# Optimization experiments

Hardware: AMD Instinct MI355X
Metric: run time of the kernel (lower is better)

Reference implementation:

```python
import jax, jax.numpy as jnp
import numpy as np

V, B, C, D, H, W = 5, 2, 32, 48, 128, 160


def setup_inputs() -> dict:
    key = jax.random.key(0)
    k1, k2, k3, k4 = jax.random.split(key, 4)
    features = jax.random.normal(k1, (V, B, C, H, W), jnp.float32)
    # Intrinsics (shared) and per-view extrinsics (identity rotation + small translation)
    K = np.eye(4, dtype=np.float32)
    K[0, 0] = 200.0; K[1, 1] = 200.0; K[0, 2] = W / 2.0; K[1, 2] = H / 2.0
    projs = np.zeros((B, V, 2, 4, 4), np.float32)
    for v in range(V):
        E = np.eye(4, dtype=np.float32)
        E[0, 3] = 0.1 * v
        E[1, 3] = 0.05 * v
        projs[:, v, 0] = E
        projs[:, v, 1] = K
    proj_matrices = jnp.asarray(projs)
    # Per-pixel depth sweep in [2, 10] with slight pixelwise perturbation
    d = jnp.linspace(2.0, 10.0, D, dtype=jnp.float32)
    depth_samples = jnp.broadcast_to(d[None, :, None, None], (B, D, H, W)) * (
        1.0 + 0.01 * jax.random.uniform(k2, (B, 1, H, W), jnp.float32))
    view_weights = jax.random.uniform(k3, (B, V - 1, H, W), jnp.float32, 0.1, 1.0)
    w_reg = 0.1 * jax.random.normal(k4, (C,), jnp.float32)
    b_reg = jnp.zeros((1,), jnp.float32)
    return {"features": features, "proj_matrices": proj_matrices,
            "depth_samples": depth_samples, "view_weights": view_weights,
            "w_reg": w_reg, "b_reg": b_reg}


def _bilinear_sample(img, px, py):
    # img: (C, H, W); px, py: (D, H, W) pixel coords. Zeros padding, align_corners=True.
    Cc, Hh, Ww = img.shape
    x0 = jnp.floor(px); y0 = jnp.floor(py)
    wx1 = px - x0; wx0 = 1.0 - wx1
    wy1 = py - y0; wy0 = 1.0 - wy1

    def gather(ix, iy, wgt):
        valid = (ix >= 0) & (ix <= Ww - 1) & (iy >= 0) & (iy <= Hh - 1)
        ixc = jnp.clip(ix, 0, Ww - 1).astype(jnp.int32)
        iyc = jnp.clip(iy, 0, Hh - 1).astype(jnp.int32)
        v = img[:, iyc, ixc]  # (C, D, H, W)
        return v * (wgt * valid)[None]

    return (gather(x0, y0, wx0 * wy0) + gather(x0 + 1, y0, wx1 * wy0)
            + gather(x0, y0 + 1, wx0 * wy1) + gather(x0 + 1, y0 + 1, wx1 * wy1))


def homo_warping(src_fea, src_proj, ref_proj, depth):
    # src_fea: (B,C,H,W); projs: (B,4,4); depth: (B,D,H,W) -> warped (B,C,D,H,W)
    Bn, Cc, Hh, Ww = src_fea.shape
    Dn = depth.shape[1]
    proj = src_proj @ jnp.linalg.inv(ref_proj)
    rot = proj[:, :3, :3]
    tr = proj[:, :3, 3]
    yy, xx = jnp.meshgrid(jnp.arange(Hh, dtype=src_fea.dtype),
                          jnp.arange(Ww, dtype=src_fea.dtype), indexing='ij')
    xyz = jnp.stack([xx.ravel(), yy.ravel(), jnp.ones(Hh * Ww, src_fea.dtype)])  # (3, HW)
    rot_xyz = jnp.einsum('bij,jn->bin', rot, xyz)  # (B, 3, HW)
    pxyz = rot_xyz[:, :, None, :] * depth.reshape(Bn, 1, Dn, Hh * Ww) + tr[:, :, None, None]
    z = pxyz[:, 2]
    valid = z > 1e-3
    zs = jnp.where(valid, z, 1.0)
    px = jnp.where(valid, pxyz[:, 0] / zs, -1e4).reshape(Bn, Dn, Hh, Ww)
    py = jnp.where(valid, pxyz[:, 1] / zs, -1e4).reshape(Bn, Dn, Hh, Ww)
    return jax.vmap(_bilinear_sample)(src_fea, px, py)


def _combined_proj(p):
    # p: (B, 2, 4, 4); new[:, :3, :4] = K[:3,:3] @ E[:3,:4]
    new = p[:, 0]
    return new.at[:, :3, :4].set(jnp.einsum('bij,bjk->bik', p[:, 1, :3, :3], p[:, 0, :3, :4]))


def reference(features, proj_matrices, depth_samples, view_weights, w_reg, b_reg):
    ref_fea = features[0]  # (B, C, H, W)
    Bn, Cc, Hh, Ww = ref_fea.shape
    Dn = depth_samples.shape[1]
    ref_proj_new = _combined_proj(proj_matrices[:, 0])
    vol_sum = jnp.zeros((Bn, Cc, Dn, Hh, Ww), ref_fea.dtype)
    wsum = jnp.full((Bn, 1, 1, Hh, Ww), 1e-5, ref_fea.dtype)
    nsrc = features.shape[0] - 1
    for i in range(nsrc):  # small fixed view loop
        src_proj_new = _combined_proj(proj_matrices[:, i + 1])
        warped = homo_warping(features[i + 1], src_proj_new, ref_proj_new, depth_samples)
        warped = warped * ref_fea[:, :, None]  # similarity volume
        w = view_weights[:, i][:, None, None]  # (B, 1, 1, H, W)
        vol_sum = vol_sum + warped * w
        wsum = wsum + w
    volume_aggregated = vol_sum / wsum
    # cost_reg_net stand-in: 1x1x1 conv over channels -> (B, D, H, W)
    prob_volume_pre = jnp.einsum('bcdhw,c->bdhw', volume_aggregated, w_reg) + b_reg
    prob_volume = jax.nn.softmax(prob_volume_pre, axis=1)
    depth = jnp.sum(prob_volume * depth_samples, axis=1)
    return (depth, jax.lax.stop_gradient(view_weights), prob_volume, volume_aggregated)
```

## Files before the change

### kernel.cpp

```cpp
#include <hip/hip_runtime.h>
#include <hip/hip_bf16.h>
#include <math.h>

#define V_ 5
#define B_ 2
#define C_ 32
#define D_ 48
#define H_ 128
#define W_ 160
#define NSRC 4
#define HW_ (H_ * W_)
#define DHW_ ((size_t)D_ * H_ * W_)
#define BHW_ (B_ * H_ * W_)
#define TOTAL_BDHW (B_ * D_ * H_ * W_)

#define NB_VOL (B_ * (H_ / 4) * (W_ / 16) * D_)
#define NB_VOL8 (NB_VOL / 8)

typedef __attribute__((ext_vector_type(2))) float f32x2;

__device__ __forceinline__ void combined_proj(const float* p, double* P) {
    double E[16], K[16];
    for (int i = 0; i < 16; ++i) { E[i] = (double)p[i]; K[i] = (double)p[16 + i]; }
    for (int i = 0; i < 16; ++i) P[i] = E[i];
    for (int r = 0; r < 3; ++r)
        for (int c = 0; c < 4; ++c) {
            double s = 0.0;
            for (int j = 0; j < 3; ++j) s += K[r * 4 + j] * E[j * 4 + c];
            P[r * 4 + c] = s;
        }
}

__device__ void invert4(const double* A, double* out) {
    double M[4][8];
    for (int r = 0; r < 4; ++r)
        for (int c = 0; c < 4; ++c) {
            M[r][c] = A[r * 4 + c];
            M[r][c + 4] = (r == c) ? 1.0 : 0.0;
        }
    for (int col = 0; col < 4; ++col) {
        int piv = col;
        double best = fabs(M[col][col]);
        for (int r = col + 1; r < 4; ++r) {
            double v = fabs(M[r][col]);
            if (v > best) { best = v; piv = r; }
        }
        if (piv != col)
            for (int c = 0; c < 8; ++c) {
                double t = M[col][c]; M[col][c] = M[piv][c]; M[piv][c] = t;
            }
        double s = 1.0 / M[col][col];
        for (int c = 0; c < 8; ++c) M[col][c] *= s;
        for (int r = 0; r < 4; ++r)
            if (r != col) {
                double f = M[r][col];
                if (f != 0.0)
                    for (int c = 0; c < 8; ++c) M[r][c] -= f * M[col][c];
            }
    }
    for (int r = 0; r < 4; ++r)
        for (int c = 0; c < 4; ++c) out[r * 4 + c] = M[r][c + 4];
}

__global__ void proj_kernel(const float* __restrict__ pm, float* __restrict__ out) {
    int t = threadIdx.x;
    if (t >= B_ * NSRC) return;
    int b = t / NSRC, i = t % NSRC;
    double Pref[16], Psrc[16];
    combined_proj(pm + (size_t)((b * V_ + 0) * 2) * 16, Pref);
    combined_proj(pm + (size_t)((b * V_ + (i + 1)) * 2) * 16, Psrc);
    double inv[16];
    invert4(Pref, inv);
    double M[16];
    for (int r = 0; r < 4; ++r)
        for (int c = 0; c < 4; ++c) {
            double s = 0.0;
            for (int j = 0; j < 4; ++j) s += Psrc[r * 4 + j] * inv[j * 4 + c];
            M[r * 4 + c] = s;
        }
    float* o = out + t * 12;
    o[0] = (float)M[0];  o[1] = (float)M[1];  o[2] = (float)M[2];
    o[3] = (float)M[4];  o[4] = (float)M[5];  o[5] = (float)M[6];
    o[6] = (float)M[8];  o[7] = (float)M[9];  o[8] = (float)M[10];
    o[9] = (float)M[3];  o[10] = (float)M[7]; o[11] = (float)M[11];
}

__global__ __launch_bounds__(256) void transpose_bf16_kernel(
    const float* __restrict__ in, __hip_bfloat16* __restrict__ outT) {
    __shared__ float tile[32][33];
    int ibh = blockIdx.x;
    int w0 = blockIdx.y * 32;
    int h = ibh % H_;
    int ib = ibh / H_;
    int i = ib / B_, b = ib % B_;
    int tx = threadIdx.x, ty = threadIdx.y;
    const float* src = in + ((size_t)((i + 1) * B_ + b) * C_) * HW_ + (size_t)h * W_ + w0;
#pragma unroll
    for (int cs = 0; cs < 32; cs += 8)
        tile[cs + ty][tx] = src[(size_t)(cs + ty) * HW_ + tx];
    __syncthreads();
    __hip_bfloat16* dst = outT + ((size_t)ib * HW_ + (size_t)h * W_ + w0) * C_;
#pragma unroll
    for (int wv = 0; wv < 32; wv += 8)
        dst[(size_t)(wv + ty) * C_ + tx] = __float2bfloat16(tile[tx][wv + ty]);
}

__global__ __launch_bounds__(256, 4) void vol_split_kernel(
    const __hip_bfloat16* __restrict__ featT, const float* __restrict__ features,
    const float* __restrict__ depth_samples, const float* __restrict__ view_weights,
    const float* __restrict__ w_reg, const float* __restrict__ b_reg,
    const float* __restrict__ projs, float* __restrict__ out_vol,
    float* __restrict__ out_pv) {
    __shared__ float lds[NSRC * 64 * 12];

    int bid = blockIdx.x;
    int lid = (bid & 7) * NB_VOL8 + (bid >> 3);
    int d = lid % D_;
    int r = lid / D_;
    int wg = r % (W_ / 16);
    r /= (W_ / 16);
    int h4 = r % (H_ / 4);
    int b = r / (H_ / 4);

    int tix = threadIdx.x;

    {
        int p = tix & 63;
        int v = tix >> 6;
        int w = wg * 16 + (p & 15);
        int h = h4 * 4 + (p >> 4);
        int pix = ((b * D_ + d) * H_ + h) * W_ + w;
        float dep = depth_samples[pix];
        float vw = view_weights[((size_t)(b * NSRC + v) * H_ + h) * W_ + w];
        const float* pr = projs + (b * NSRC + v) * 12;
        float xf = (float)w, yf = (float)h;
        float rx = pr[0] * xf + pr[1] * yf + pr[2];
        float ry = pr[3] * xf + pr[4] * yf + pr[5];
        float rz = pr[6] * xf + pr[7] * yf + pr[8];
        float pxn = rx * dep + pr[9];
        float pyn = ry * dep + pr[10];
        float z = rz * dep + pr[11];
        bool valid = z > 0.001f;
        float zr = __builtin_amdgcn_rcpf(valid ? z : 1.f);
        float px = valid ? pxn * zr : -10000.f;
        float py = valid ? pyn * zr : -10000.f;

        float x0f = floorf(px), y0f = floorf(py);
        float wx1 = px - x0f, wx0 = 1.f - wx1;
        float wy1 = py - y0f, wy0 = 1.f - wy1;
        bool vx0 = (x0f >= 0.f) && (x0f <= (float)(W_ - 1));
        bool vx1 = (x0f >= -1.f) && (x0f <= (float)(W_ - 2));
        bool vy0 = (y0f >= 0.f) && (y0f <= (float)(H_ - 1));
        bool vy1 = (y0f >= -1.f) && (y0f <= (float)(H_ - 2));
        int ix0 = (int)fminf(fmaxf(x0f, 0.f), (float)(W_ - 1));
        int ix1 = (int)fminf(fmaxf(x0f + 1.f, 0.f), (float)(W_ - 1));
        int iy0 = (int)fminf(fmaxf(y0f, 0.f), (float)(H_ - 1));
        int iy1 = (int)fminf(fmaxf(y0f + 1.f, 0.f), (float)(H_ - 1));
        float w00 = wx0 * wy0 * ((vx0 && vy0) ? vw : 0.f);
        float w10 = wx1 * wy0 * ((vx1 && vy0) ? vw : 0.f);
        float w01 = wx0 * wy1 * ((vx0 && vy1) ? vw : 0.f);
        float w11 = wx1 * wy1 * ((vx1 && vy1) ? vw : 0.f);

        int o00 = (iy0 * W_ + ix0) << 6;
        int o10 = (iy0 * W_ + ix1) << 6;
        int o01 = (iy1 * W_ + ix0) << 6;
        int o11 = (iy1 * W_ + ix1) << 6;

        float* row = lds + (size_t)((v << 6) + p) * 12;
        *(float4*)row = make_float4(w00, w10, w01, w11);
        *(int4*)(row + 4) = make_int4(o00, o10, o01, o11);
        row[8] = vw;
    }
    __syncthreads();

    int w16 = tix & 15;
    int c4 = (tix >> 4) & 3;
    int hg = tix >> 6;
    int p = w16 + 16 * hg;
    int h = h4 * 4 + hg;
    int w = wg * 16 + w16;
    int c0 = c4 * 8;
    int c16 = c4 * 16;

    float4 wv4[NSRC];
    int4 ov[NSRC];
    float vws[NSRC];
#pragma unroll
    for (int v = 0; v < NSRC; ++v) {
        const float* row = lds + (size_t)((v << 6) + p) * 12;
        wv4[v] = *(const float4*)row;
        ov[v] = *(const int4*)(row + 4);
        vws[v] = row[8];
    }
    float wsum = 1e-5f + vws[0] + vws[1] + vws[2] + vws[3];

    uint4 u[NSRC][4];
#pragma unroll
    for (int v = 0; v < NSRC; ++v) {
        const char* fv = (const char*)(featT + (size_t)(v * B_ + b) * HW_ * C_) + c16;
        u[v][0] = *(const uint4*)(fv + ov[v].x);
        u[v][1] = *(const uint4*)(fv + ov[v].y);
        u[v][2] = *(const uint4*)(fv + ov[v].z);
        u[v][3] = *(const uint4*)(fv + ov[v].w);
    }

    const float* refp = features + ((size_t)b * C_ + c0) * HW_ + (size_t)h * W_ + w;
    float refv[8];
#pragma unroll
    for (int k = 0; k < 8; ++k) refv[k] = refp[(size_t)k * HW_];

    __builtin_amdgcn_sched_barrier(0);

    f32x2 acc[4];
#pragma unroll
    for (int j = 0; j < 4; ++j) acc[j] = (f32x2){0.f, 0.f};

#define ACCPK(word, j, wgt)                                              \
    {                                                                    \
        f32x2 t;                                                         \
        t.x = __uint_as_float((word) << 16);                             \
        t.y = __uint_as_float((word) & 0xffff0000u);                     \
        acc[j] += t * (wgt);                                             \
    }
#pragma unroll
    for (int v = 0; v < NSRC; ++v) {
        f32x2 wv;
#define ACCTAP(uu, wcomp)                                                \
        wv = (f32x2){wcomp, wcomp};                                      \
        ACCPK((uu).x, 0, wv)                                             \
        ACCPK((uu).y, 1, wv)                                             \
        ACCPK((uu).z, 2, wv)                                             \
        ACCPK((uu).w, 3, wv)
        ACCTAP(u[v][0], wv4[v].x)
        ACCTAP(u[v][1], wv4[v].y)
        ACCTAP(u[v][2], wv4[v].z)
        ACCTAP(u[v][3], wv4[v].w)
#undef ACCTAP
    }
#undef ACCPK

    float inv_wsum = __builtin_amdgcn_rcpf(wsum);
    int pix_idx = ((b * D_ + d) * H_ + h) * W_ + w;
    size_t obase = (size_t)b * C_ * DHW_ + (size_t)d * HW_ + (size_t)h * W_ + w;
    float4 wr0 = *(const float4*)(w_reg + c0);
    float4 wr1 = *(const float4*)(w_reg + c0 + 4);
    float wrr[8] = {wr0.x, wr0.y, wr0.z, wr0.w, wr1.x, wr1.y, wr1.z, wr1.w};
    float pv = 0.f;
#pragma unroll
    for (int k = 0; k < 8; ++k) {
        float vc = refv[k] * acc[k >> 1][k & 1] * inv_wsum;
        __builtin_nontemporal_store(vc, &out_vol[obase + (size_t)(c0 + k) * DHW_]);
        pv += vc * wrr[k];
    }
    pv += __shfl_xor(pv, 16, 64);
    pv += __shfl_xor(pv, 32, 64);
    if (c4 == 0) out_pv[pix_idx] = pv + b_reg[0];
}

__global__ __launch_bounds__(256) void vol_fallback_kernel(
    const float* __restrict__ feat, const float* __restrict__ depth_samples,
    const float* __restrict__ view_weights, const float* __restrict__ w_reg,
    const float* __restrict__ b_reg, const float* __restrict__ projs,
    float* __restrict__ out_vol, float* __restrict__ out_pv) {
    int tid = blockIdx.x * 256 + threadIdx.x;
    if (tid >= TOTAL_BDHW) return;
    int w = tid % W_;
    int t2 = tid / W_;
    int h = t2 % H_;
    t2 /= H_;
    int d = t2 % D_;
    int b = t2 / D_;

    float xf = (float)w, yf = (float)h;
    float dep = depth_samples[tid];
    float s[C_];
#pragma unroll
    for (int c = 0; c < C_; ++c) s[c] = 0.f;
    float wsum = 1e-5f;

    for (int i = 0; i < NSRC; ++i) {
        float vw = view_weights[((size_t)(b * NSRC + i) * H_ + h) * W_ + w];
        wsum += vw;
        const float* pr = projs + (b * NSRC + i) * 12;
        float rx = pr[0] * xf + pr[1] * yf + pr[2];
        float ry = pr[3] * xf + pr[4] * yf + pr[5];
        float rz = pr[6] * xf + pr[7] * yf + pr[8];
        float pxn = rx * dep + pr[9];
        float pyn = ry * dep + pr[10];
        float z = rz * dep + pr[11];
        bool valid = z > 0.001f;
        float zs = valid ? z : 1.f;
        float px = valid ? pxn / zs : -10000.f;
        float py = valid ? pyn / zs : -10000.f;
        float x0f = floorf(px), y0f = floorf(py);
        float x1f = x0f + 1.f, y1f = y0f + 1.f;
        float wx1 = px - x0f, wx0 = 1.f - wx1;
        float wy1 = py - y0f, wy0 = 1.f - wy1;
        bool vx0 = (x0f >= 0.f) && (x0f <= (float)(W_ - 1));
        bool vx1 = (x1f >= 0.f) && (x1f <= (float)(W_ - 1));
        bool vy0 = (y0f >= 0.f) && (y0f <= (float)(H_ - 1));
        bool vy1 = (y1f >= 0.f) && (y1f <= (float)(H_ - 1));
        int ix0 = (int)fminf(fmaxf(x0f, 0.f), (float)(W_ - 1));
        int ix1 = (int)fminf(fmaxf(x1f, 0.f), (float)(W_ - 1));
        int iy0 = (int)fminf(fmaxf(y0f, 0.f), (float)(H_ - 1));
        int iy1 = (int)fminf(fmaxf(y1f, 0.f), (float)(H_ - 1));
        float w00 = wx0 * wy0 * ((vx0 && vy0) ? vw : 0.f);
        float w10 = wx1 * wy0 * ((vx1 && vy0) ? vw : 0.f);
        float w01 = wx0 * wy1 * ((vx0 && vy1) ? vw : 0.f);
        float w11 = wx1 * wy1 * ((vx1 && vy1) ? vw : 0.f);
// ... 37 lines not shown
#pragma unroll
    for (int d = 0; d < D_; ++d) {
        p[d] = pv[base + (size_t)d * HW_];
        m = fmaxf(m, p[d]);
    }
    float ssum = 0.f;
#pragma unroll
    for (int d = 0; d < D_; ++d) {
        p[d] = expf(p[d] - m);
        ssum += p[d];
    }
    float inv = 1.f / ssum;
    float dep = 0.f;
#pragma unroll
    for (int d = 0; d < D_; ++d) {
        float pr = p[d] * inv;
        pv[base + (size_t)d * HW_] = pr;
        dep += pr * ds[base + (size_t)d * HW_];
    }
    out_depth[tid] = dep;
#pragma unroll
    for (int k = 0; k < NSRC; ++k)
        out_vw[tid + k * BHW_] = vw[tid + k * BHW_];
}

extern "C" void kernel_launch(void* const* d_in, const int* in_sizes, int n_in,
                              void* d_out, int out_size, void* d_ws, size_t ws_size,
                              hipStream_t stream) {
    const float* features = (const float*)d_in[0];
    const float* pm       = (const float*)d_in[1];
    const float* dsamp    = (const float*)d_in[2];
    const float* vweights = (const float*)d_in[3];
    const float* w_reg    = (const float*)d_in[4];
    const float* b_reg    = (const float*)d_in[5];

    float* out = (float*)d_out;
    float* out_depth = out;
    float* out_vw    = out + 40960;
    float* out_prob  = out + 204800;
    float* out_vol   = out + 2170880;

    float* wsf   = (float*)d_ws;
    float* projb = wsf;
    __hip_bfloat16* featT = (__hip_bfloat16*)(wsf + 128);

    size_t need = 512 + (size_t)NSRC * B_ * HW_ * C_ * sizeof(__hip_bfloat16);
    bool chlast = (ws_size >= need);

    hipLaunchKernelGGL(proj_kernel, dim3(1), dim3(64), 0, stream, pm, projb);

    if (chlast) {
        hipLaunchKernelGGL(transpose_bf16_kernel, dim3(NSRC * B_ * H_, W_ / 32),
                           dim3(32, 8), 0, stream, features, featT);
        hipLaunchKernelGGL(vol_split_kernel, dim3(NB_VOL), dim3(256), 0, stream,
                           featT, features, dsamp, vweights, w_reg, b_reg, projb,
                           out_vol, out_prob);
    } else {
        hipLaunchKernelGGL(vol_fallback_kernel, dim3((TOTAL_BDHW + 255) / 256),
                           dim3(256), 0, stream, features, dsamp, vweights, w_reg,
                           b_reg, projb, out_vol, out_prob);
    }

    hipLaunchKernelGGL(finalize_kernel, dim3(BHW_ / 256), dim3(256), 0, stream,
                       dsamp, vweights, out_depth, out_vw, out_prob);
}
```

Before: 169.7 us.

## Loop over depth inside each block with double-buffered LDS sampling rows

Replaces the one-block-per-depth-slice volume kernel with a kernel where each block handles half the depth range for a 4x16 pixel tile. Per-pixel setup (projection ray, view weight, reference features, w_reg, weight-sum reciprocal) is hoisted out of the depth loop and reused. Sampling rows for the next depth are computed into a second LDS buffer while the current depth is gathered. The grid shrinks from roughly 30k blocks to 1280, which cuts redundant loads and block launch overhead but lowers parallelism and adds a barrier per depth step.

```diff
diff --git a/kernel.cpp b/kernel.cpp
--- a/kernel.cpp
+++ b/kernel.cpp
@@ -14,8 +14,9 @@
 #define BHW_ (B_ * H_ * W_)
 #define TOTAL_BDHW (B_ * D_ * H_ * W_)
 
-#define NB_VOL (B_ * (H_ / 4) * (W_ / 16) * D_)
-#define NB_VOL8 (NB_VOL / 8)
+#define DHALF (D_ / 2)
+#define NB_DLOOP (B_ * (H_ / 4) * (W_ / 16) * 2)
+#define NB_DLOOP8 (NB_DLOOP / 8)
 
 typedef __attribute__((ext_vector_type(2))) float f32x2;
 
@@ -105,156 +106,195 @@
         dst[(size_t)(wv + ty) * C_ + tx] = __float2bfloat16(tile[tx][wv + ty]);
 }
 
-__global__ __launch_bounds__(256, 4) void vol_split_kernel(
+__device__ __forceinline__ void make_row(float dep, float rx, float ry, float rz,
+                                         float t9, float t10, float t11, float vw,
+                                         float* __restrict__ row) {
+    float pxn = rx * dep + t9;
+    float pyn = ry * dep + t10;
+    float z = rz * dep + t11;
+    bool valid = z > 0.001f;
+    float zr = __builtin_amdgcn_rcpf(valid ? z : 1.f);
+    float px = valid ? pxn * zr : -10000.f;
+    float py = valid ? pyn * zr : -10000.f;
+
+    float x0f = floorf(px), y0f = floorf(py);
+    float wx1 = px - x0f, wx0 = 1.f - wx1;
+    float wy1 = py - y0f, wy0 = 1.f - wy1;
+    bool vx0 = (x0f >= 0.f) && (x0f <= (float)(W_ - 1));
+    bool vx1 = (x0f >= -1.f) && (x0f <= (float)(W_ - 2));
+    bool vy0 = (y0f >= 0.f) && (y0f <= (float)(H_ - 1));
+    bool vy1 = (y0f >= -1.f) && (y0f <= (float)(H_ - 2));
+    int ix0 = (int)fminf(fmaxf(x0f, 0.f), (float)(W_ - 1));
+    int ix1 = (int)fminf(fmaxf(x0f + 1.f, 0.f), (float)(W_ - 1));
+    int iy0 = (int)fminf(fmaxf(y0f, 0.f), (float)(H_ - 1));
+    int iy1 = (int)fminf(fmaxf(y0f + 1.f, 0.f), (float)(H_ - 1));
+    float w00 = wx0 * wy0 * ((vx0 && vy0) ? vw : 0.f);
+    float w10 = wx1 * wy0 * ((vx1 && vy0) ? vw : 0.f);
+    float w01 = wx0 * wy1 * ((vx0 && vy1) ? vw : 0.f);
+    float w11 = wx1 * wy1 * ((vx1 && vy1) ? vw : 0.f);
+
+    int o00 = (iy0 * W_ + ix0) << 6;
+    int o10 = (iy0 * W_ + ix1) << 6;
+    int o01 = (iy1 * W_ + ix0) << 6;
+    int o11 = (iy1 * W_ + ix1) << 6;
+
+    *(float4*)row = make_float4(w00, w10, w01, w11);
+    *(int4*)(row + 4) = make_int4(o00, o10, o01, o11);
+    row[8] = vw;
+}
+
+__global__ __launch_bounds__(256, 4) void vol_dloop_kernel(
     const __hip_bfloat16* __restrict__ featT, const float* __restrict__ features,
     const float* __restrict__ depth_samples, const float* __restrict__ view_weights,
     const float* __restrict__ w_reg, const float* __restrict__ b_reg,
     const float* __restrict__ projs, float* __restrict__ out_vol,
     float* __restrict__ out_pv) {
-    __shared__ float lds[NSRC * 64 * 12];
+    __shared__ float lds[2][NSRC * 64 * 12];
 
     int bid = blockIdx.x;
-    int lid = (bid & 7) * NB_VOL8 + (bid >> 3);
-    int d = lid % D_;
-    int r = lid / D_;
-    int wg = r % (W_ / 16);
-    r /= (W_ / 16);
-    int h4 = r % (H_ / 4);
-    int b = r / (H_ / 4);
+    int lid = (bid & 7) * NB_DLOOP8 + (bid >> 3);
+    int dhalf = lid & 1;
+    int t = lid >> 1;
+    int wg = t % (W_ / 16);
+    t /= (W_ / 16);
+    int h4 = t % (H_ / 4);
+    int b = t / (H_ / 4);
+    int d0 = dhalf * DHALF;
 
     int tix = threadIdx.x;
 
-    {
-        int p = tix & 63;
-        int v = tix >> 6;
-        int w = wg * 16 + (p & 15);
-        int h = h4 * 4 + (p >> 4);
-        int pix = ((b * D_ + d) * H_ + h) * W_ + w;
-        float dep = depth_samples[pix];
-        float vw = view_weights[((size_t)(b * NSRC + v) * H_ + h) * W_ + w];
-        const float* pr = projs + (b * NSRC + v) * 12;
-        float xf = (float)w, yf = (float)h;
-        float rx = pr[0] * xf + pr[1] * yf + pr[2];
-        float ry = pr[3] * xf + pr[4] * yf + pr[5];
-        float rz = pr[6] * xf + pr[7] * yf + pr[8];
-        float pxn = rx * dep + pr[9];
-        float pyn = ry * dep + pr[10];
-        float z = rz * dep + pr[11];
-        bool valid = z > 0.001f;
-        float zr = __builtin_amdgcn_rcpf(valid ? z : 1.f);
-        float px = valid ? pxn * zr : -10000.f;
-        float py = valid ? pyn * zr : -10000.f;
-
-        float x0f = floorf(px), y0f = floorf(py);
-        float wx1 = px - x0f, wx0 = 1.f - wx1;
-        float wy1 = py - y0f, wy0 = 1.f - wy1;
-        bool vx0 = (x0f >= 0.f) && (x0f <= (float)(W_ - 1));
-        bool vx1 = (x0f >= -1.f) && (x0f <= (float)(W_ - 2));
-        bool vy0 = (y0f >= 0.f) && (y0f <= (float)(H_ - 1));
-        bool vy1 = (y0f >= -1.f) && (y0f <= (float)(H_ - 2));
-        int ix0 = (int)fminf(fmaxf(x0f, 0.f), (float)(W_ - 1));
-        int ix1 = (int)fminf(fmaxf(x0f + 1.f, 0.f), (float)(W_ - 1));
-        int iy0 = (int)fminf(fmaxf(y0f, 0.f), (float)(H_ - 1));
-        int iy1 = (int)fminf(fmaxf(y0f + 1.f, 0.f), (float)(H_ - 1));
-        float w00 = wx0 * wy0 * ((vx0 && vy0) ? vw : 0.f);
-        float w10 = wx1 * wy0 * ((vx1 && vy0) ? vw : 0.f);
-        float w01 = wx0 * wy1 * ((vx0 && vy1) ? vw : 0.f);
-        float w11 = wx1 * wy1 * ((vx1 && vy1) ? vw : 0.f);
-
-        int o00 = (iy0 * W_ + ix0) << 6;
-        int o10 = (iy0 * W_ + ix1) << 6;
-        int o01 = (iy1 * W_ + ix0) << 6;
-        int o11 = (iy1 * W_ + ix1) << 6;
-
-        float* row = lds + (size_t)((v << 6) + p) * 12;
-        *(float4*)row = make_float4(w00, w10, w01, w11);
-        *(int4*)(row + 4) = make_int4(o00, o10, o01, o11);
-        row[8] = vw;
-    }
-    __syncthreads();
+    int p1 = tix & 63;
+    int v1 = tix >> 6;
+    int w1 = wg * 16 + (p1 & 15);
+    int h1 = h4 * 4 + (p1 >> 4);
+    const float* pr = projs + (b * NSRC + v1) * 12;
+    float xf = (float)w1, yf = (float)h1;
+    float rx = pr[0] * xf + pr[1] * yf + pr[2];
+    float ry = pr[3] * xf + pr[4] * yf + pr[5];
+    float rz = pr[6] * xf + pr[7] * yf + pr[8];
+    float t9 = pr[9], t10 = pr[10], t11 = pr[11];
+    float vw1 = view_weights[((size_t)(b * NSRC + v1) * H_ + h1) * W_ + w1];
+    int dspix1 = (b * D_) * HW_ + h1 * W_ + w1;
+    float* row0 = &lds[0][(size_t)((v1 << 6) + p1) * 12];
+    float* row1 = &lds[1][(size_t)((v1 << 6) + p1) * 12];
 
     int w16 = tix & 15;
     int c4 = (tix >> 4) & 3;
     int hg = tix >> 6;
-    int p = w16 + 16 * hg;
-    int h = h4 * 4 + hg;
-    int w = wg * 16 + w16;
+    int p2 = w16 + 16 * hg;
+    int h2 = h4 * 4 + hg;
+    int w2 = wg * 16 + w16;
     int c0 = c4 * 8;
-    int c16 = c4 * 16;
-
-    float4 wv4[NSRC];
-    int4 ov[NSRC];
-    float vws[NSRC];
-#pragma unroll
-    for (int v = 0; v < NSRC; ++v) {
-        const float* row = lds + (size_t)((v << 6) + p) * 12;
-        wv4[v] = *(const float4*)row;
-        ov[v] = *(const int4*)(row + 4);
-        vws[v] = row[8];
-    }
-    float wsum = 1e-5f + vws[0] + vws[1] + vws[2] + vws[3];
-
-    uint4 u[NSRC][4];
-#pragma unroll
-    for (int v = 0; v < NSRC; ++v) {
-        const char* fv = (const char*)(featT + (size_t)(v * B_ + b) * HW_ * C_) + c16;
-        u[v][0] = *(const uint4*)(fv + ov[v].x);
-        u[v][1] = *(const uint4*)(fv + ov[v].y);
-        u[v][2] = *(const uint4*)(fv + ov[v].z);
-        u[v][3] = *(const uint4*)(fv + ov[v].w);
-    }
-
-    const float* refp = features + ((size_t)b * C_ + c0) * HW_ + (size_t)h * W_ + w;
+    int c16b = c4 * 16;
+    const char* fv0 = (const char*)(featT + (size_t)(0 * B_ + b) * HW_ * C_) + c16b;
+    const char* fv1 = (const char*)(featT + (size_t)(1 * B_ + b) * HW_ * C_) + c16b;
+    const char* fv2 = (const char*)(featT + (size_t)(2 * B_ + b) * HW_ * C_) + c16b;
+    const char* fv3 = (const char*)(featT + (size_t)(3 * B_ + b) * HW_ * C_) + c16b;
+    const float* rbase0 = &lds[0][(size_t)p2 * 12];
+    const float* rbase1 = &lds[1][(size_t)p2 * 12];
+
+    const float* refp = features + ((size_t)b * C_ + c0) * HW_ + (size_t)h2 * W_ + w2;
     float refv[8];
 #pragma unroll
     for (int k = 0; k < 8; ++k) refv[k] = refp[(size_t)k * HW_];
-
-    __builtin_amdgcn_sched_barrier(0);
-
-    f32x2 acc[4];
-#pragma unroll
-    for (int j = 0; j < 4; ++j) acc[j] = (f32x2){0.f, 0.f};
-
-#define ACCPK(word, j, wgt)                                              \
-    {                                                                    \
-        f32x2 t;                                                         \
-        t.x = __uint_as_float((word) << 16);                             \
-        t.y = __uint_as_float((word) & 0xffff0000u);                     \
-        acc[j] += t * (wgt);                                             \
-    }
-#pragma unroll
-    for (int v = 0; v < NSRC; ++v) {
-        f32x2 wv;
-#define ACCTAP(uu, wcomp)                                                \
-        wv = (f32x2){wcomp, wcomp};                                      \
-        ACCPK((uu).x, 0, wv)                                             \
-        ACCPK((uu).y, 1, wv)                                             \
-        ACCPK((uu).z, 2, wv)                                             \
-        ACCPK((uu).w, 3, wv)
-        ACCTAP(u[v][0], wv4[v].x)
-        ACCTAP(u[v][1], wv4[v].y)
-        ACCTAP(u[v][2], wv4[v].z)
-        ACCTAP(u[v][3], wv4[v].w)
-#undef ACCTAP
-    }
-#undef ACCPK
-
-    float inv_wsum = __builtin_amdgcn_rcpf(wsum);
-    int pix_idx = ((b * D_ + d) * H_ + h) * W_ + w;
-    size_t obase = (size_t)b * C_ * DHW_ + (size_t)d * HW_ + (size_t)h * W_ + w;
     float4 wr0 = *(const float4*)(w_reg + c0);
     float4 wr1 = *(const float4*)(w_reg + c0 + 4);
     float wrr[8] = {wr0.x, wr0.y, wr0.z, wr0.w, wr1.x, wr1.y, wr1.z, wr1.w};
-    float pv = 0.f;
-#pragma unroll
-    for (int k = 0; k < 8; ++k) {
-        float vc = refv[k] * acc[k >> 1][k & 1] * inv_wsum;
-        __builtin_nontemporal_store(vc, &out_vol[obase + (size_t)(c0 + k) * DHW_]);
-        pv += vc * wrr[k];
-    }
-    pv += __shfl_xor(pv, 16, 64);
-    pv += __shfl_xor(pv, 32, 64);
-    if (c4 == 0) out_pv[pix_idx] = pv + b_reg[0];
+    float breg = b_reg[0];
+    size_t obase0 = (size_t)b * C_ * DHW_ + (size_t)h2 * W_ + w2;
+    int pvpix0 = (b * D_) * HW_ + h2 * W_ + w2;
+    float inv_wsum = 0.f;
+
+    {
+        float dep = depth_samples[dspix1 + d0 * HW_];
+        make_row(dep, rx, ry, rz, t9, t10, t11, vw1, row0);
+    }
+    __syncthreads();
+
+    for (int di = 0; di < DHALF; ++di) {
+        int d = d0 + di;
+        if (di + 1 < DHALF) {
+            float dep = depth_samples[dspix1 + (d + 1) * HW_];
+            make_row(dep, rx, ry, rz, t9, t10, t11, vw1,
+                     ((di + 1) & 1) ? row1 : row0);
+        }
+
+        const float* rb = (di & 1) ? rbase1 : rbase0;
+        float4 wv4[NSRC];
+        int4 ov[NSRC];
+#pragma unroll
+        for (int v = 0; v < NSRC; ++v) {
+            const float* row = rb + (size_t)(v << 6) * 12;
+            wv4[v] = *(const float4*)row;
+            ov[v] = *(const int4*)(row + 4);
+        }
+        if (di == 0) {
+            float wsum = 1e-5f;
+#pragma unroll
+            for (int v = 0; v < NSRC; ++v) wsum += (rb + (size_t)(v << 6) * 12)[8];
+            inv_wsum = __builtin_amdgcn_rcpf(wsum);
+        }
+
+        uint4 u[NSRC][4];
+        u[0][0] = *(const uint4*)(fv0 + ov[0].x);
+        u[0][1] = *(const uint4*)(fv0 + ov[0].y);
+        u[0][2] = *(const uint4*)(fv0 + ov[0].z);
+        u[0][3] = *(const uint4*)(fv0 + ov[0].w);
+        u[1][0] = *(const uint4*)(fv1 + ov[1].x);
+        u[1][1] = *(const uint4*)(fv1 + ov[1].y);
+        u[1][2] = *(const uint4*)(fv1 + ov[1].z);
+        u[1][3] = *(const uint4*)(fv1 + ov[1].w);
+        u[2][0] = *(const uint4*)(fv2 + ov[2].x);
+        u[2][1] = *(const uint4*)(fv2 + ov[2].y);
+        u[2][2] = *(const uint4*)(fv2 + ov[2].z);
+        u[2][3] = *(const uint4*)(fv2 + ov[2].w);
+        u[3][0] = *(const uint4*)(fv3 + ov[3].x);
+        u[3][1] = *(const uint4*)(fv3 + ov[3].y);
+        u[3][2] = *(const uint4*)(fv3 + ov[3].z);
+        u[3][3] = *(const uint4*)(fv3 + ov[3].w);
+
+        f32x2 acc[4];
+#pragma unroll
+        for (int j = 0; j < 4; ++j) acc[j] = (f32x2){0.f, 0.f};
+
+#define ACCPK(word, j, wgt)                                              \
+        {                                                                \
+            f32x2 tt;                                                    \
+            tt.x = __uint_as_float((word) << 16);                        \
+            tt.y = __uint_as_float((word) & 0xffff0000u);                \
+            acc[j] += tt * (wgt);                                        \
+        }
+#pragma unroll
+        for (int v = 0; v < NSRC; ++v) {
+            f32x2 wv;
+#define ACCTAP(uu, wcomp)                                                \
+            wv = (f32x2){wcomp, wcomp};                                  \
+            ACCPK((uu).x, 0, wv)                                         \
+            ACCPK((uu).y, 1, wv)                                         \
+            ACCPK((uu).z, 2, wv)                                         \
+            ACCPK((uu).w, 3, wv)
+            ACCTAP(u[v][0], wv4[v].x)
+            ACCTAP(u[v][1], wv4[v].y)
+            ACCTAP(u[v][2], wv4[v].z)
+            ACCTAP(u[v][3], wv4[v].w)
+#undef ACCTAP
+        }
+#undef ACCPK
+
+        size_t obase = obase0 + (size_t)d * HW_;
+        float pv = 0.f;
+#pragma unroll
+        for (int k = 0; k < 8; ++k) {
+            float vc = refv[k] * acc[k >> 1][k & 1] * inv_wsum;
+            __builtin_nontemporal_store(vc, &out_vol[obase + (size_t)(c0 + k) * DHW_]);
+            pv += vc * wrr[k];
+        }
+        pv += __shfl_xor(pv, 16, 64);
+        pv += __shfl_xor(pv, 32, 64);
+        if (c4 == 0) out_pv[pvpix0 + d * HW_] = pv + breg;
+
+        __syncthreads();
+    }
 }
 
 __global__ __launch_bounds__(256) void vol_fallback_kernel(
@@ -398,7 +438,7 @@
     if (chlast) {
         hipLaunchKernelGGL(transpose_bf16_kernel, dim3(NSRC * B_ * H_, W_ / 32),
                            dim3(32, 8), 0, stream, features, featT);
-        hipLaunchKernelGGL(vol_split_kernel, dim3(NB_VOL), dim3(256), 0, stream,
+        hipLaunchKernelGGL(vol_dloop_kernel, dim3(NB_DLOOP), dim3(256), 0, stream,
                            featT, features, dsamp, vweights, w_reg, b_reg, projb,
                            out_vol, out_prob);
     } else {
```

New measurement: 174.7 us. 1.03x slower.

## Process two depth planes per block to reuse reference features and view setup

Applied to the files above, without the earlier changes.

Each block of the volume kernel now handles a pair of depth slices instead of one, so the grid is half the size. The reference-feature loads, view weights, projection rays, w_reg and the 1/wsum scaling are loaded or computed once and shared by both slices. All 32 bf16 gathers for both slices are issued before any accumulation to expose more memory parallelism. The cost is higher register use (launch bounds drop from 4 to 2 blocks per CU), doubled LDS per block and fewer blocks, which may lower occupancy for this memory-bound kernel.

```diff
diff --git a/kernel.cpp b/kernel.cpp
--- a/kernel.cpp
+++ b/kernel.cpp
@@ -14,8 +14,9 @@
 #define BHW_ (B_ * H_ * W_)
 #define TOTAL_BDHW (B_ * D_ * H_ * W_)
 
-#define NB_VOL (B_ * (H_ / 4) * (W_ / 16) * D_)
-#define NB_VOL8 (NB_VOL / 8)
+#define DPAIR (D_ / 2)
+#define NB_PAIR (B_ * (H_ / 4) * (W_ / 16) * DPAIR)
+#define NB_PAIR8 (NB_PAIR / 8)
 
 typedef __attribute__((ext_vector_type(2))) float f32x2;
 
@@ -105,22 +106,61 @@
         dst[(size_t)(wv + ty) * C_ + tx] = __float2bfloat16(tile[tx][wv + ty]);
 }
 
-__global__ __launch_bounds__(256, 4) void vol_split_kernel(
+__device__ __forceinline__ void make_row(float dep, float rx, float ry, float rz,
+                                         float t9, float t10, float t11, float vw,
+                                         float* __restrict__ row) {
+    float pxn = rx * dep + t9;
+    float pyn = ry * dep + t10;
+    float z = rz * dep + t11;
+    bool valid = z > 0.001f;
+    float zr = __builtin_amdgcn_rcpf(valid ? z : 1.f);
+    float px = valid ? pxn * zr : -10000.f;
+    float py = valid ? pyn * zr : -10000.f;
+
+    float x0f = floorf(px), y0f = floorf(py);
+    float wx1 = px - x0f, wx0 = 1.f - wx1;
+    float wy1 = py - y0f, wy0 = 1.f - wy1;
+    bool vx0 = (x0f >= 0.f) && (x0f <= (float)(W_ - 1));
+    bool vx1 = (x0f >= -1.f) && (x0f <= (float)(W_ - 2));
+    bool vy0 = (y0f >= 0.f) && (y0f <= (float)(H_ - 1));
+    bool vy1 = (y0f >= -1.f) && (y0f <= (float)(H_ - 2));
+    int ix0 = (int)fminf(fmaxf(x0f, 0.f), (float)(W_ - 1));
+    int ix1 = (int)fminf(fmaxf(x0f + 1.f, 0.f), (float)(W_ - 1));
+    int iy0 = (int)fminf(fmaxf(y0f, 0.f), (float)(H_ - 1));
+    int iy1 = (int)fminf(fmaxf(y0f + 1.f, 0.f), (float)(H_ - 1));
+    float w00 = wx0 * wy0 * ((vx0 && vy0) ? vw : 0.f);
+    float w10 = wx1 * wy0 * ((vx1 && vy0) ? vw : 0.f);
+    float w01 = wx0 * wy1 * ((vx0 && vy1) ? vw : 0.f);
+    float w11 = wx1 * wy1 * ((vx1 && vy1) ? vw : 0.f);
+
+    int o00 = (iy0 * W_ + ix0) << 6;
+    int o10 = (iy0 * W_ + ix1) << 6;
+    int o01 = (iy1 * W_ + ix0) << 6;
+    int o11 = (iy1 * W_ + ix1) << 6;
+
+    *(float4*)row = make_float4(w00, w10, w01, w11);
+    *(int4*)(row + 4) = make_int4(o00, o10, o01, o11);
+    row[8] = vw;
+}
+
+__global__ __launch_bounds__(256, 2) void vol_pair_kernel(
     const __hip_bfloat16* __restrict__ featT, const float* __restrict__ features,
     const float* __restrict__ depth_samples, const float* __restrict__ view_weights,
     const float* __restrict__ w_reg, const float* __restrict__ b_reg,
     const float* __restrict__ projs, float* __restrict__ out_vol,
     float* __restrict__ out_pv) {
-    __shared__ float lds[NSRC * 64 * 12];
+    __shared__ float lds[2][NSRC * 64 * 12];
 
     int bid = blockIdx.x;
-    int lid = (bid & 7) * NB_VOL8 + (bid >> 3);
-    int d = lid % D_;
-    int r = lid / D_;
+    int lid = (bid & 7) * NB_PAIR8 + (bid >> 3);
+    int dp = lid % DPAIR;
+    int r = lid / DPAIR;
     int wg = r % (W_ / 16);
     r /= (W_ / 16);
     int h4 = r % (H_ / 4);
     int b = r / (H_ / 4);
+    int d0 = dp * 2;
+    int d1 = d0 + 1;
 
     int tix = threadIdx.x;
 
@@ -129,132 +169,147 @@
         int v = tix >> 6;
         int w = wg * 16 + (p & 15);
         int h = h4 * 4 + (p >> 4);
-        int pix = ((b * D_ + d) * H_ + h) * W_ + w;
-        float dep = depth_samples[pix];
+        int pixbase = (b * D_) * HW_ + h * W_ + w;
         float vw = view_weights[((size_t)(b * NSRC + v) * H_ + h) * W_ + w];
         const float* pr = projs + (b * NSRC + v) * 12;
         float xf = (float)w, yf = (float)h;
         float rx = pr[0] * xf + pr[1] * yf + pr[2];
         float ry = pr[3] * xf + pr[4] * yf + pr[5];
         float rz = pr[6] * xf + pr[7] * yf + pr[8];
-        float pxn = rx * dep + pr[9];
-        float pyn = ry * dep + pr[10];
-        float z = rz * dep + pr[11];
-        bool valid = z > 0.001f;
-        float zr = __builtin_amdgcn_rcpf(valid ? z : 1.f);
-        float px = valid ? pxn * zr : -10000.f;
-        float py = valid ? pyn * zr : -10000.f;
-
-        float x0f = floorf(px), y0f = floorf(py);
-        float wx1 = px - x0f, wx0 = 1.f - wx1;
-        float wy1 = py - y0f, wy0 = 1.f - wy1;
-        bool vx0 = (x0f >= 0.f) && (x0f <= (float)(W_ - 1));
-        bool vx1 = (x0f >= -1.f) && (x0f <= (float)(W_ - 2));
-        bool vy0 = (y0f >= 0.f) && (y0f <= (float)(H_ - 1));
-        bool vy1 = (y0f >= -1.f) && (y0f <= (float)(H_ - 2));
-        int ix0 = (int)fminf(fmaxf(x0f, 0.f), (float)(W_ - 1));
-        int ix1 = (int)fminf(fmaxf(x0f + 1.f, 0.f), (float)(W_ - 1));
-        int iy0 = (int)fminf(fmaxf(y0f, 0.f), (float)(H_ - 1));
-        int iy1 = (int)fminf(fmaxf(y0f + 1.f, 0.f), (float)(H_ - 1));
-        float w00 = wx0 * wy0 * ((vx0 && vy0) ? vw : 0.f);
-        float w10 = wx1 * wy0 * ((vx1 && vy0) ? vw : 0.f);
-        float w01 = wx0 * wy1 * ((vx0 && vy1) ? vw : 0.f);
-        float w11 = wx1 * wy1 * ((vx1 && vy1) ? vw : 0.f);
-
-        int o00 = (iy0 * W_ + ix0) << 6;
-        int o10 = (iy0 * W_ + ix1) << 6;
-        int o01 = (iy1 * W_ + ix0) << 6;
-        int o11 = (iy1 * W_ + ix1) << 6;
-
-        float* row = lds + (size_t)((v << 6) + p) * 12;
-        *(float4*)row = make_float4(w00, w10, w01, w11);
-        *(int4*)(row + 4) = make_int4(o00, o10, o01, o11);
-        row[8] = vw;
+        float t9 = pr[9], t10 = pr[10], t11 = pr[11];
+        float dep0 = depth_samples[pixbase + d0 * HW_];
+        float dep1 = depth_samples[pixbase + d1 * HW_];
+        float* row = &lds[0][(size_t)((v << 6) + p) * 12];
+        make_row(dep0, rx, ry, rz, t9, t10, t11, vw, row);
+        make_row(dep1, rx, ry, rz, t9, t10, t11, vw,
+                 &lds[1][(size_t)((v << 6) + p) * 12]);
     }
     __syncthreads();
 
     int w16 = tix & 15;
     int c4 = (tix >> 4) & 3;
     int hg = tix >> 6;
-    int p = w16 + 16 * hg;
-    int h = h4 * 4 + hg;
-    int w = wg * 16 + w16;
+    int p2 = w16 + 16 * hg;
+    int h2 = h4 * 4 + hg;
+    int w2 = wg * 16 + w16;
     int c0 = c4 * 8;
-    int c16 = c4 * 16;
-
-    float4 wv4[NSRC];
-    int4 ov[NSRC];
+    int c16b = c4 * 16;
+
+    float4 wv4a[NSRC], wv4b[NSRC];
+    int4 ova[NSRC], ovb[NSRC];
     float vws[NSRC];
 #pragma unroll
     for (int v = 0; v < NSRC; ++v) {
-        const float* row = lds + (size_t)((v << 6) + p) * 12;
-        wv4[v] = *(const float4*)row;
-        ov[v] = *(const int4*)(row + 4);
-        vws[v] = row[8];
+        const float* rowa = &lds[0][(size_t)((v << 6) + p2) * 12];
+        const float* rowb = &lds[1][(size_t)((v << 6) + p2) * 12];
+        wv4a[v] = *(const float4*)rowa;
+        ova[v] = *(const int4*)(rowa + 4);
+        vws[v] = rowa[8];
+        wv4b[v] = *(const float4*)rowb;
+        ovb[v] = *(const int4*)(rowb + 4);
     }
     float wsum = 1e-5f + vws[0] + vws[1] + vws[2] + vws[3];
-
-    uint4 u[NSRC][4];
-#pragma unroll
-    for (int v = 0; v < NSRC; ++v) {
-        const char* fv = (const char*)(featT + (size_t)(v * B_ + b) * HW_ * C_) + c16;
-        u[v][0] = *(const uint4*)(fv + ov[v].x);
-        u[v][1] = *(const uint4*)(fv + ov[v].y);
-        u[v][2] = *(const uint4*)(fv + ov[v].z);
-        u[v][3] = *(const uint4*)(fv + ov[v].w);
-    }
-
-    const float* refp = features + ((size_t)b * C_ + c0) * HW_ + (size_t)h * W_ + w;
+    float inv_wsum = __builtin_amdgcn_rcpf(wsum);
+
+    const char* fv0 = (const char*)(featT + (size_t)(0 * B_ + b) * HW_ * C_) + c16b;
+    const char* fv1 = (const char*)(featT + (size_t)(1 * B_ + b) * HW_ * C_) + c16b;
+    const char* fv2 = (const char*)(featT + (size_t)(2 * B_ + b) * HW_ * C_) + c16b;
+    const char* fv3 = (const char*)(featT + (size_t)(3 * B_ + b) * HW_ * C_) + c16b;
+    uint4 ua[NSRC][4], ub[NSRC][4];
+#define G4(dst, fv, ovv)                                                 \
+    dst[0] = *(const uint4*)((fv) + (ovv).x);                            \
+    dst[1] = *(const uint4*)((fv) + (ovv).y);                            \
+    dst[2] = *(const uint4*)((fv) + (ovv).z);                            \
+    dst[3] = *(const uint4*)((fv) + (ovv).w);
+    G4(ua[0], fv0, ova[0]) G4(ua[1], fv1, ova[1])
+    G4(ua[2], fv2, ova[2]) G4(ua[3], fv3, ova[3])
+    G4(ub[0], fv0, ovb[0]) G4(ub[1], fv1, ovb[1])
+    G4(ub[2], fv2, ovb[2]) G4(ub[3], fv3, ovb[3])
+#undef G4
+
+    const float* refp = features + ((size_t)b * C_ + c0) * HW_ + (size_t)h2 * W_ + w2;
     float refv[8];
 #pragma unroll
     for (int k = 0; k < 8; ++k) refv[k] = refp[(size_t)k * HW_];
+    float4 wr0 = *(const float4*)(w_reg + c0);
+    float4 wr1 = *(const float4*)(w_reg + c0 + 4);
+    float breg = b_reg[0];
 
     __builtin_amdgcn_sched_barrier(0);
 
-    f32x2 acc[4];
-#pragma unroll
-    for (int j = 0; j < 4; ++j) acc[j] = (f32x2){0.f, 0.f};
+    float wrr[8] = {wr0.x, wr0.y, wr0.z, wr0.w, wr1.x, wr1.y, wr1.z, wr1.w};
+    float refs[8];
+#pragma unroll
+    for (int k = 0; k < 8; ++k) refs[k] = refv[k] * inv_wsum;
 
 #define ACCPK(word, j, wgt)                                              \
     {                                                                    \
-        f32x2 t;                                                         \
-        t.x = __uint_as_float((word) << 16);                             \
-        t.y = __uint_as_float((word) & 0xffff0000u);                     \
-        acc[j] += t * (wgt);                                             \
-    }
-#pragma unroll
-    for (int v = 0; v < NSRC; ++v) {
-        f32x2 wv;
+        f32x2 tt;                                                        \
+        tt.x = __uint_as_float((word) << 16);                            \
+        tt.y = __uint_as_float((word) & 0xffff0000u);                    \
+        acc[j] += tt * (wgt);                                            \
+    }
 #define ACCTAP(uu, wcomp)                                                \
-        wv = (f32x2){wcomp, wcomp};                                      \
+    {                                                                    \
+        f32x2 wv = (f32x2){wcomp, wcomp};                                \
         ACCPK((uu).x, 0, wv)                                             \
         ACCPK((uu).y, 1, wv)                                             \
         ACCPK((uu).z, 2, wv)                                             \
-        ACCPK((uu).w, 3, wv)
-        ACCTAP(u[v][0], wv4[v].x)
-        ACCTAP(u[v][1], wv4[v].y)
-        ACCTAP(u[v][2], wv4[v].z)
-        ACCTAP(u[v][3], wv4[v].w)
+        ACCPK((uu).w, 3, wv)                                             \
+    }
+
+    size_t obase0 = (size_t)b * C_ * DHW_ + (size_t)h2 * W_ + w2;
+    int pvpix = (b * D_) * HW_ + h2 * W_ + w2;
+
+    {
+        f32x2 acc[4];
+#pragma unroll
+        for (int j = 0; j < 4; ++j) acc[j] = (f32x2){0.f, 0.f};
+#pragma unroll
+        for (int v = 0; v < NSRC; ++v) {
+            ACCTAP(ua[v][0], wv4a[v].x)
+            ACCTAP(ua[v][1], wv4a[v].y)
+            ACCTAP(ua[v][2], wv4a[v].z)
+            ACCTAP(ua[v][3], wv4a[v].w)
+        }
+        size_t obase = obase0 + (size_t)d0 * HW_;
+        float pv = 0.f;
+#pragma unroll
+        for (int k = 0; k < 8; ++k) {
+            float vc = refs[k] * acc[k >> 1][k & 1];
+            __builtin_nontemporal_store(vc, &out_vol[obase + (size_t)(c0 + k) * DHW_]);
+            pv += vc * wrr[k];
+        }
+        pv += __shfl_xor(pv, 16, 64);
+        pv += __shfl_xor(pv, 32, 64);
+        if (c4 == 0) out_pv[pvpix + d0 * HW_] = pv + breg;
+    }
+
+    {
+        f32x2 acc[4];
+#pragma unroll
+        for (int j = 0; j < 4; ++j) acc[j] = (f32x2){0.f, 0.f};
+#pragma unroll
+        for (int v = 0; v < NSRC; ++v) {
+            ACCTAP(ub[v][0], wv4b[v].x)
+            ACCTAP(ub[v][1], wv4b[v].y)
+            ACCTAP(ub[v][2], wv4b[v].z)
+            ACCTAP(ub[v][3], wv4b[v].w)
+        }
+        size_t obase = obase0 + (size_t)d1 * HW_;
+        float pv = 0.f;
+#pragma unroll
+        for (int k = 0; k < 8; ++k) {
+            float vc = refs[k] * acc[k >> 1][k & 1];
+            __builtin_nontemporal_store(vc, &out_vol[obase + (size_t)(c0 + k) * DHW_]);
+            pv += vc * wrr[k];
+        }
+        pv += __shfl_xor(pv, 16, 64);
+        pv += __shfl_xor(pv, 32, 64);
+        if (c4 == 0) out_pv[pvpix + d1 * HW_] = pv + breg;
+    }
 #undef ACCTAP
-    }
 #undef ACCPK
-
-    float inv_wsum = __builtin_amdgcn_rcpf(wsum);
-    int pix_idx = ((b * D_ + d) * H_ + h) * W_ + w;
-    size_t obase = (size_t)b * C_ * DHW_ + (size_t)d * HW_ + (size_t)h * W_ + w;
-    float4 wr0 = *(const float4*)(w_reg + c0);
-    float4 wr1 = *(const float4*)(w_reg + c0 + 4);
-    float wrr[8] = {wr0.x, wr0.y, wr0.z, wr0.w, wr1.x, wr1.y, wr1.z, wr1.w};
-    float pv = 0.f;
-#pragma unroll
-    for (int k = 0; k < 8; ++k) {
-        float vc = refv[k] * acc[k >> 1][k & 1] * inv_wsum;
-        __builtin_nontemporal_store(vc, &out_vol[obase + (size_t)(c0 + k) * DHW_]);
-        pv += vc * wrr[k];
-    }
-    pv += __shfl_xor(pv, 16, 64);
-    pv += __shfl_xor(pv, 32, 64);
-    if (c4 == 0) out_pv[pix_idx] = pv + b_reg[0];
 }
 
 __global__ __launch_bounds__(256) void vol_fallback_kernel(
@@ -398,7 +453,7 @@
     if (chlast) {
         hipLaunchKernelGGL(transpose_bf16_kernel, dim3(NSRC * B_ * H_, W_ / 32),
                            dim3(32, 8), 0, stream, features, featT);
-        hipLaunchKernelGGL(vol_split_kernel, dim3(NB_VOL), dim3(256), 0, stream,
+        hipLaunchKernelGGL(vol_pair_kernel, dim3(NB_PAIR), dim3(256), 0, stream,
                            featT, features, dsamp, vweights, w_reg, b_reg, projb,
                            out_vol, out_prob);
     } else {
```

Measured after the change: 194.6 us. 14.7% more time.

## Stage per-view bilinear source footprint box in LDS before gathering

Applied to the files above, without the earlier changes.

Each block computes, via wave reductions, the bounding box of the source pixels that its 64 reference pixels project to in each view. When that box fits in 20x8 pixels, the bf16 channels-last features inside it are copied cooperatively into LDS, and the bilinear gathers then read from LDS rather than doing scattered global loads. The aim is to replace uncoalesced global gathers with coalesced box loads plus cheap LDS reads. In exchange the kernel uses about 40KB of LDS, occupancy drops to 3 blocks per CU, and it adds an extra barrier and may load box pixels that are never used.

```diff
diff --git a/kernel.cpp b/kernel.cpp
--- a/kernel.cpp
+++ b/kernel.cpp
@@ -16,6 +16,10 @@
 
 #define NB_VOL (B_ * (H_ / 4) * (W_ / 16) * D_)
 #define NB_VOL8 (NB_VOL / 8)
+
+#define CAPX 20
+#define CAPY 8
+#define BOXB (CAPX * CAPY * 64)
 
 typedef __attribute__((ext_vector_type(2))) float f32x2;
 
@@ -105,13 +109,15 @@
         dst[(size_t)(wv + ty) * C_ + tx] = __float2bfloat16(tile[tx][wv + ty]);
 }
 
-__global__ __launch_bounds__(256, 4) void vol_split_kernel(
+__global__ __launch_bounds__(256, 3) void vol_box_kernel(
     const __hip_bfloat16* __restrict__ featT, const float* __restrict__ features,
     const float* __restrict__ depth_samples, const float* __restrict__ view_weights,
     const float* __restrict__ w_reg, const float* __restrict__ b_reg,
     const float* __restrict__ projs, float* __restrict__ out_vol,
     float* __restrict__ out_pv) {
-    __shared__ float lds[NSRC * 64 * 12];
+    __shared__ float wrow[NSRC][64][12];
+    __shared__ int4 boxmeta[NSRC];
+    __shared__ __align__(16) char boxes[NSRC][BOXB];
 
     int bid = blockIdx.x;
     int lid = (bid & 7) * NB_VOL8 + (bid >> 3);
@@ -145,105 +151,145 @@
         float px = valid ? pxn * zr : -10000.f;
         float py = valid ? pyn * zr : -10000.f;
 
-        float x0f = floorf(px), y0f = floorf(py);
-        float wx1 = px - x0f, wx0 = 1.f - wx1;
-        float wy1 = py - y0f, wy0 = 1.f - wy1;
-        bool vx0 = (x0f >= 0.f) && (x0f <= (float)(W_ - 1));
-        bool vx1 = (x0f >= -1.f) && (x0f <= (float)(W_ - 2));
-        bool vy0 = (y0f >= 0.f) && (y0f <= (float)(H_ - 1));
-        bool vy1 = (y0f >= -1.f) && (y0f <= (float)(H_ - 2));
-        int ix0 = (int)fminf(fmaxf(x0f, 0.f), (float)(W_ - 1));
-        int ix1 = (int)fminf(fmaxf(x0f + 1.f, 0.f), (float)(W_ - 1));
-        int iy0 = (int)fminf(fmaxf(y0f, 0.f), (float)(H_ - 1));
-        int iy1 = (int)fminf(fmaxf(y0f + 1.f, 0.f), (float)(H_ - 1));
+        float fx = floorf(px), fy = floorf(py);
+
+        float fxmin = fx, fxmax = fx, fymin = fy, fymax = fy;
+#pragma unroll
+        for (int m = 1; m < 64; m <<= 1) {
+            fxmin = fminf(fxmin, __shfl_xor(fxmin, m, 64));
+            fxmax = fmaxf(fxmax, __shfl_xor(fxmax, m, 64));
+            fymin = fminf(fymin, __shfl_xor(fymin, m, 64));
+            fymax = fmaxf(fymax, __shfl_xor(fymax, m, 64));
+        }
+        int cx0 = min(max((int)fxmin, 0), W_ - 1);
+        int cx1 = min(max((int)fxmax + 1, 0), W_ - 1);
+        int cy0 = min(max((int)fymin, 0), H_ - 1);
+        int cy1 = min(max((int)fymax + 1, 0), H_ - 1);
+        int bw = cx1 - cx0 + 1, bh = cy1 - cy0 + 1;
+        bool fits = (bw <= CAPX) && (bh <= CAPY);
+
+        float wx1 = px - fx, wx0 = 1.f - wx1;
+        float wy1 = py - fy, wy0 = 1.f - wy1;
+        bool vx0 = (fx >= 0.f) && (fx <= (float)(W_ - 1));
+        bool vx1 = (fx >= -1.f) && (fx <= (float)(W_ - 2));
+        bool vy0 = (fy >= 0.f) && (fy <= (float)(H_ - 1));
+        bool vy1 = (fy >= -1.f) && (fy <= (float)(H_ - 2));
+        int ix0 = min(max((int)fx, 0), W_ - 1);
+        int ix1 = min(max((int)fx + 1, 0), W_ - 1);
+        int iy0 = min(max((int)fy, 0), H_ - 1);
+        int iy1 = min(max((int)fy + 1, 0), H_ - 1);
         float w00 = wx0 * wy0 * ((vx0 && vy0) ? vw : 0.f);
         float w10 = wx1 * wy0 * ((vx1 && vy0) ? vw : 0.f);
         float w01 = wx0 * wy1 * ((vx0 && vy1) ? vw : 0.f);
         float w11 = wx1 * wy1 * ((vx1 && vy1) ? vw : 0.f);
 
-        int o00 = (iy0 * W_ + ix0) << 6;
-        int o10 = (iy0 * W_ + ix1) << 6;
-        int o01 = (iy1 * W_ + ix0) << 6;
-        int o11 = (iy1 * W_ + ix1) << 6;
-
-        float* row = lds + (size_t)((v << 6) + p) * 12;
+        int o00, o10, o01, o11;
+        if (fits) {
+            o00 = ((iy0 - cy0) * CAPX + (ix0 - cx0)) << 6;
+            o10 = ((iy0 - cy0) * CAPX + (ix1 - cx0)) << 6;
+            o01 = ((iy1 - cy0) * CAPX + (ix0 - cx0)) << 6;
+            o11 = ((iy1 - cy0) * CAPX + (ix1 - cx0)) << 6;
+        } else {
+            o00 = (iy0 * W_ + ix0) << 6;
+            o10 = (iy0 * W_ + ix1) << 6;
+            o01 = (iy1 * W_ + ix0) << 6;
+            o11 = (iy1 * W_ + ix1) << 6;
+        }
+        float* row = &wrow[v][p][0];
         *(float4*)row = make_float4(w00, w10, w01, w11);
         *(int4*)(row + 4) = make_int4(o00, o10, o01, o11);
         row[8] = vw;
+        if (p == 0) boxmeta[v] = make_int4(cx0, cy0, bw, fits ? bh : 0);
+    }
+    __syncthreads();
+
+#pragma unroll
+    for (int v = 0; v < NSRC; ++v) {
+        int4 mv = boxmeta[v];
+        int bh2 = mv.w;
+        if (bh2 > 0) {
+            int nq = bh2 * (CAPX * 4);
+            const char* fvb = (const char*)(featT + (size_t)(v * B_ + b) * HW_ * C_);
+            for (int q = tix; q < nq; q += 256) {
+                int rrow = q / (CAPX * 4);
+                int c = q - rrow * (CAPX * 4);
+                int col = min(mv.x + (c >> 2), W_ - 1);
+                uint4 val = *(const uint4*)(fvb + ((((mv.y + rrow) * W_ + col) << 6) + ((c & 3) << 4)));
+                *(uint4*)(&boxes[v][0] + (q << 4)) = val;
+            }
+        }
     }
     __syncthreads();
 
     int w16 = tix & 15;
     int c4 = (tix >> 4) & 3;
     int hg = tix >> 6;
-    int p = w16 + 16 * hg;
-    int h = h4 * 4 + hg;
-    int w = wg * 16 + w16;
+    int p2 = w16 + 16 * hg;
+    int h2 = h4 * 4 + hg;
+    int w2 = wg * 16 + w16;
     int c0 = c4 * 8;
-    int c16 = c4 * 16;
-
-    float4 wv4[NSRC];
-    int4 ov[NSRC];
-    float vws[NSRC];
-#pragma unroll
-    for (int v = 0; v < NSRC; ++v) {
-        const float* row = lds + (size_t)((v << 6) + p) * 12;
-        wv4[v] = *(const float4*)row;
-        ov[v] = *(const int4*)(row + 4);
-        vws[v] = row[8];
-    }
-    float wsum = 1e-5f + vws[0] + vws[1] + vws[2] + vws[3];
-
-    uint4 u[NSRC][4];
-#pragma unroll
-    for (int v = 0; v < NSRC; ++v) {
-        const char* fv = (const char*)(featT + (size_t)(v * B_ + b) * HW_ * C_) + c16;
-        u[v][0] = *(const uint4*)(fv + ov[v].x);
-        u[v][1] = *(const uint4*)(fv + ov[v].y);
-        u[v][2] = *(const uint4*)(fv + ov[v].z);
-        u[v][3] = *(const uint4*)(fv + ov[v].w);
-    }
-
-    const float* refp = features + ((size_t)b * C_ + c0) * HW_ + (size_t)h * W_ + w;
+    int c16b = c4 * 16;
+
+    const float* refp = features + ((size_t)b * C_ + c0) * HW_ + (size_t)h2 * W_ + w2;
     float refv[8];
 #pragma unroll
     for (int k = 0; k < 8; ++k) refv[k] = refp[(size_t)k * HW_];
-
-    __builtin_amdgcn_sched_barrier(0);
-
+    float4 wr0 = *(const float4*)(w_reg + c0);
+    float4 wr1 = *(const float4*)(w_reg + c0 + 4);
+    float breg = b_reg[0];
+
+    float wsum = 1e-5f;
     f32x2 acc[4];
 #pragma unroll
     for (int j = 0; j < 4; ++j) acc[j] = (f32x2){0.f, 0.f};
 
 #define ACCPK(word, j, wgt)                                              \
     {                                                                    \
-        f32x2 t;                                                         \
-        t.x = __uint_as_float((word) << 16);                             \
-        t.y = __uint_as_float((word) & 0xffff0000u);                     \
-        acc[j] += t * (wgt);                                             \
-    }
-#pragma unroll
-    for (int v = 0; v < NSRC; ++v) {
-        f32x2 wv;
+        f32x2 tt;                                                        \
+        tt.x = __uint_as_float((word) << 16);                            \
+        tt.y = __uint_as_float((word) & 0xffff0000u);                    \
+        acc[j] += tt * (wgt);                                            \
+    }
 #define ACCTAP(uu, wcomp)                                                \
-        wv = (f32x2){wcomp, wcomp};                                      \
+    {                                                                    \
+        f32x2 wv = (f32x2){wcomp, wcomp};                                \
         ACCPK((uu).x, 0, wv)                                             \
         ACCPK((uu).y, 1, wv)                                             \
         ACCPK((uu).z, 2, wv)                                             \
-        ACCPK((uu).w, 3, wv)
-        ACCTAP(u[v][0], wv4[v].x)
-        ACCTAP(u[v][1], wv4[v].y)
-        ACCTAP(u[v][2], wv4[v].z)
-        ACCTAP(u[v][3], wv4[v].w)
+        ACCPK((uu).w, 3, wv)                                             \
+    }
+
+#pragma unroll
+    for (int v = 0; v < NSRC; ++v) {
+        const float* row = &wrow[v][p2][0];
+        float4 wv4 = *(const float4*)row;
+        int4 ov = *(const int4*)(row + 4);
+        wsum += row[8];
+        uint4 u0, u1, u2, u3;
+        if (boxmeta[v].w > 0) {
+            const char* lb = &boxes[v][0] + c16b;
+            u0 = *(const uint4*)(lb + ov.x);
+            u1 = *(const uint4*)(lb + ov.y);
+            u2 = *(const uint4*)(lb + ov.z);
+            u3 = *(const uint4*)(lb + ov.w);
+        } else {
+            const char* fv = (const char*)(featT + (size_t)(v * B_ + b) * HW_ * C_) + c16b;
+            u0 = *(const uint4*)(fv + ov.x);
+            u1 = *(const uint4*)(fv + ov.y);
+            u2 = *(const uint4*)(fv + ov.z);
+            u3 = *(const uint4*)(fv + ov.w);
+        }
+        ACCTAP(u0, wv4.x)
+        ACCTAP(u1, wv4.y)
+        ACCTAP(u2, wv4.z)
+        ACCTAP(u3, wv4.w)
+    }
 #undef ACCTAP
-    }
 #undef ACCPK
 
     float inv_wsum = __builtin_amdgcn_rcpf(wsum);
-    int pix_idx = ((b * D_ + d) * H_ + h) * W_ + w;
-    size_t obase = (size_t)b * C_ * DHW_ + (size_t)d * HW_ + (size_t)h * W_ + w;
-    float4 wr0 = *(const float4*)(w_reg + c0);
-    float4 wr1 = *(const float4*)(w_reg + c0 + 4);
+    int pix_idx = ((b * D_ + d) * H_ + h2) * W_ + w2;
+    size_t obase = (size_t)b * C_ * DHW_ + (size_t)d * HW_ + (size_t)h2 * W_ + w2;
     float wrr[8] = {wr0.x, wr0.y, wr0.z, wr0.w, wr1.x, wr1.y, wr1.z, wr1.w};
     float pv = 0.f;
 #pragma unroll
@@ -254,7 +300,7 @@
     }
     pv += __shfl_xor(pv, 16, 64);
     pv += __shfl_xor(pv, 32, 64);
-    if (c4 == 0) out_pv[pix_idx] = pv + b_reg[0];
+    if (c4 == 0) out_pv[pix_idx] = pv + breg;
 }
 
 __global__ __launch_bounds__(256) void vol_fallback_kernel(
@@ -398,7 +444,7 @@
     if (chlast) {
         hipLaunchKernelGGL(transpose_bf16_kernel, dim3(NSRC * B_ * H_, W_ / 32),
                            dim3(32, 8), 0, stream, features, featT);
-        hipLaunchKernelGGL(vol_split_kernel, dim3(NB_VOL), dim3(256), 0, stream,
+        hipLaunchKernelGGL(vol_box_kernel, dim3(NB_VOL), dim3(256), 0, stream,
                            featT, features, dsamp, vweights, w_reg, b_reg, projb,
                            out_vol, out_prob);
     } else {
```

After: 233.1 us. 1.37x slower.
